# Kernel tuning notes

Measured on AMD Instinct MI355X. Metric: run time of the kernel, lower is better.

Reference implementation:

```python
import jax, jax.numpy as jnp
import numpy as np

B, DV, W, H = 64, 2048, 14, 14
DQ, DA, G, DH, NC = 2400, 1200, 2, 1200, 3000


def setup_inputs() -> dict:
    key = jax.random.key(0)
    ks = jax.random.split(key, 14)
    s = lambda k, shp, scale=0.02: jax.random.normal(k, shp, dtype=jnp.float32) * scale
    return {
        "input_q": jax.random.normal(ks[0], (B, DQ), dtype=jnp.float32),
        "input_v": jax.random.normal(ks[1], (B, DV, W, H), dtype=jnp.float32),
        "Wv_att": s(ks[2], (DA, DV)),
        "bv_att": s(ks[3], (DA,)),
        "Wq_att": s(ks[4], (DA, DQ)),
        "bq_att": s(ks[5], (DA,)),
        "Watt": s(ks[6], (G, DA)),
        "batt": s(ks[7], (G,)),
        "Wv_fus": s(ks[8], (G, DH, DV)),
        "bv_fus": s(ks[9], (G, DH)),
        "Wq_fus": s(ks[10], (G * DH, DQ)),
        "bq_fus": s(ks[11], (G * DH,)),
        "Wc": s(ks[12], (NC, G * DH)),
        "bc": s(ks[13], (NC,)),
    }


def reference(input_q, input_v, Wv_att, bv_att, Wq_att, bq_att, Watt, batt,
              Wv_fus, bv_fus, Wq_fus, bq_fus, Wc, bc):
    b, dv, w, h = input_v.shape
    n = w * h  # spatial positions

    # --- attention branch (eval mode: dropout = identity) ---
    # 1x1 conv == per-position linear over channels; activation_v = tanh
    xv = jnp.tanh(jnp.einsum('bchw,dc->bdhw', input_v, Wv_att) + bv_att[None, :, None, None])
    xv = xv.reshape(b, -1, n).transpose(0, 2, 1)               # [B, WH, DA]
    # question projection; activation_q = tanh
    xq = jnp.tanh(input_q @ Wq_att.T + bq_att)                 # [B, DA]
    # MLB Hadamard fusion + activation_mm = tanh
    xatt = jnp.tanh(xv * xq[:, None, :])                       # [B, WH, DA]
    # glimpse scores: 1x1 conv over dim_mm channels
    wgt = jnp.einsum('bnd,gd->bgn', xatt, Watt) + batt[None, :, None]  # [B, G, WH]
    att = jax.nn.softmax(wgt, axis=-1)                         # softmax over WH per glimpse

    # weighted sum of ORIGINAL features per glimpse
    v_flat = input_v.reshape(b, dv, n)                         # [B, DV, WH]
    v_att = jnp.einsum('bgn,bdn->bgd', att, v_flat)            # [B, G, DV]

    # --- glimpse fusion + classification ---
    v_fus = jnp.tanh(jnp.einsum('bgd,ghd->bgh', v_att, Wv_fus) + bv_fus)  # [B, G, DH]
    v_fus = v_fus.reshape(b, -1)                               # [B, G*DH] (concat over glimpses)
    q_fus = jnp.tanh(input_q @ Wq_fus.T + bq_fus)              # [B, G*DH]
    x = (v_fus * q_fus) @ Wc.T + bc                            # [B, NC]
    return (x, wgt)
```

## Files before the change

kernel.cpp:

```cpp
#include <hip/hip_runtime.h>
#include <hip/hip_fp16.h>

typedef _Float16 half8 __attribute__((ext_vector_type(8)));
typedef float f32x4 __attribute__((ext_vector_type(4)));

__device__ __forceinline__ float tanh_fast(float x) {
  float e = __expf(2.0f * x);
  return 1.0f - 2.0f / (e + 1.0f);
}

__device__ __forceinline__ void gload16(const _Float16* g, _Float16* l) {
  __builtin_amdgcn_global_load_lds((const __attribute__((address_space(1))) void*)g,
                                   (__attribute__((address_space(3))) void*)l,
                                   16, 0, 0);
}

__global__ __launch_bounds__(256) void k_transpose_v(const float* __restrict__ in,
                                                     _Float16* __restrict__ out) {
  __shared__ float t[64][65];
  int b = blockIdx.z;
  int c0 = blockIdx.y * 64;
  int p0 = blockIdx.x * 64;
  int tid = threadIdx.x;
  int pl = tid & 63;
  #pragma unroll
  for (int s = 0; s < 16; ++s) {
    int cl = (tid >> 6) + s * 4;
    int p = p0 + pl;
    t[cl][pl] = (p < 196) ? in[((size_t)b * 2048 + (c0 + cl)) * 196 + p] : 0.0f;
  }
  __syncthreads();
  int c8 = (tid & 7) * 8;
  #pragma unroll
  for (int s = 0; s < 2; ++s) {
    int p = p0 + (tid >> 3) + s * 32;
    if (p < 196) {
      half8 v;
      #pragma unroll
      for (int j = 0; j < 8; ++j) v[j] = (_Float16)t[c8 + j][(tid >> 3) + s * 32];
      *(half8*)(out + ((size_t)b * 196 + p) * 2048 + c0 + c8) = v;
    }
  }
}

__global__ __launch_bounds__(256) void k_prep(const float* __restrict__ W,
                                              _Float16* __restrict__ Wh,
                                              const float* __restrict__ batt,
                                              float* __restrict__ wgt) {
  int i = blockIdx.x * 256 + threadIdx.x;
  int n = i >> 11;
  Wh[i] = (n < 1200) ? (_Float16)W[i] : (_Float16)0.0f;
  if (i < 25088) wgt[i] = batt[(i / 196) & 1];
}

__global__ __launch_bounds__(256) void k_gemm1(const _Float16* __restrict__ A,
                                               const _Float16* __restrict__ B,
                                               const float* __restrict__ bias,
                                               const float* __restrict__ xq,
                                               const float* __restrict__ Watt,
                                               float* __restrict__ wgt) {
  __shared__ __align__(16) _Float16 As[128 * 64];
  __shared__ __align__(16) _Float16 Bs[128 * 64];
  int tid = threadIdx.x;
  int n0 = blockIdx.x * 128;
  int m0 = blockIdx.y * 128;
  int lane = tid & 63;
  int wave = tid >> 6;
  int wm = (wave >> 1) * 64;
  int wn = (wave & 1) * 64;
  int fr = lane & 15;
  int fq = lane >> 4;

  int rsub = lane >> 3;
  int gchunk = (lane & 7) ^ rsub;
  const _Float16* aSrc = A + (size_t)(m0 + wave * 8 + rsub) * 2048 + gchunk * 8;
  const _Float16* bSrc = B + (size_t)(n0 + wave * 8 + rsub) * 2048 + gchunk * 8;
  _Float16* aDst = As + (wave * 8) * 64;
  _Float16* bDst = Bs + (wave * 8) * 64;

  f32x4 acc[4][4];
  #pragma unroll
  for (int i = 0; i < 4; ++i)
    #pragma unroll
    for (int j = 0; j < 4; ++j) acc[i][j] = (f32x4){0.f, 0.f, 0.f, 0.f};

  for (int kt = 0; kt < 32; ++kt) {
    int k0 = kt * 64;
    __syncthreads();
    #pragma unroll
    for (int j = 0; j < 4; ++j) {
      gload16(aSrc + k0 + (size_t)j * 32 * 2048, aDst + j * 32 * 64);
      gload16(bSrc + k0 + (size_t)j * 32 * 2048, bDst + j * 32 * 64);
    }
    __syncthreads();
    #pragma unroll
    for (int s = 0; s < 2; ++s) {
      half8 af[4], bf[4];
      #pragma unroll
      for (int mt = 0; mt < 4; ++mt) {
        int row = wm + mt * 16 + fr;
        af[mt] = *(const half8*)(As + row * 64 + (((s * 4 + fq) ^ (fr & 7)) << 3));
      }
      #pragma unroll
      for (int nt = 0; nt < 4; ++nt) {
        int row = wn + nt * 16 + fr;
        bf[nt] = *(const half8*)(Bs + row * 64 + (((s * 4 + fq) ^ (fr & 7)) << 3));
      }
      #pragma unroll
      for (int mt = 0; mt < 4; ++mt)
        #pragma unroll
        for (int nt = 0; nt < 4; ++nt)
          acc[mt][nt] = __builtin_amdgcn_mfma_f32_16x16x32_f16(af[mt], bf[nt], acc[mt][nt], 0, 0, 0);
    }
  }

  float s0[16], s1[16];
  #pragma unroll
  for (int i = 0; i < 16; ++i) { s0[i] = 0.f; s1[i] = 0.f; }

  #pragma unroll
  for (int nt = 0; nt < 4; ++nt) {
    int col = n0 + wn + nt * 16 + fr;
    bool ok = col < 1200;
    float bcol = ok ? bias[col] : 0.f;
    float wa0 = ok ? Watt[col] : 0.f;
    float wa1 = ok ? Watt[1200 + col] : 0.f;
    #pragma unroll
    for (int mt = 0; mt < 4; ++mt) {
      #pragma unroll
      for (int r = 0; r < 4; ++r) {
        int row = m0 + wm + mt * 16 + fq * 4 + r;
        int b = row / 196;
        float xqv = ok ? xq[b * 1200 + col] : 0.f;
        float xv = tanh_fast(acc[mt][nt][r] + bcol);
        float xa = tanh_fast(xv * xqv);
        s0[mt * 4 + r] += xa * wa0;
        s1[mt * 4 + r] += xa * wa1;
      }
    }
  }
  #pragma unroll
  for (int i = 0; i < 16; ++i) {
    #pragma unroll
    for (int off = 8; off > 0; off >>= 1) {
      s0[i] += __shfl_down(s0[i], off);
      s1[i] += __shfl_down(s1[i], off);
    }
  }
  if (fr == 0) {
    #pragma unroll
    for (int i = 0; i < 16; ++i) {
      int row = m0 + wm + (i >> 2) * 16 + fq * 4 + (i & 3);
      int b = row / 196;
      int p = row - b * 196;
      atomicAdd(&wgt[(b * 2 + 0) * 196 + p], s0[i]);
      atomicAdd(&wgt[(b * 2 + 1) * 196 + p], s1[i]);
    }
  }
}

__global__ __launch_bounds__(64) void k_softmax(const float* __restrict__ wgt,
                                                float* __restrict__ att) {
  int bg = blockIdx.x;
  int lane = threadIdx.x;
  const float* wr = wgt + (size_t)bg * 196;
  float v[4];
  #pragma unroll
  for (int i = 0; i < 4; ++i) {
    int n = lane + i * 64;
    v[i] = (n < 196) ? wr[n] : -1e30f;
  }
  float mx = fmaxf(fmaxf(v[0], v[1]), fmaxf(v[2], v[3]));
  #pragma unroll
  for (int off = 32; off > 0; off >>= 1) mx = fmaxf(mx, __shfl_xor(mx, off));
  float s = 0.f;
  #pragma unroll
  for (int i = 0; i < 4; ++i) {
    int n = lane + i * 64;
    float e = (n < 196) ? __expf(v[i] - mx) : 0.f;
    v[i] = e;
    s += e;
  }
  #pragma unroll
  for (int off = 32; off > 0; off >>= 1) s += __shfl_xor(s, off);
  float inv = 1.f / s;
  #pragma unroll
  for (int i = 0; i < 4; ++i) {
    int n = lane + i * 64;
    if (n < 196) att[(size_t)bg * 196 + n] = v[i] * inv;
  }
}

__global__ __launch_bounds__(256) void k_vatt(const _Float16* __restrict__ Vt,
                                              const float* __restrict__ att,
                                              float* __restrict__ v_att) {
  __shared__ float a0s[196], a1s[196];
  int b = blockIdx.y;
  int tid = threadIdx.x;
  if (tid < 196) {
    a0s[tid] = att[((size_t)b * 2 + 0) * 196 + tid];
    a1s[tid] = att[((size_t)b * 2 + 1) * 196 + tid];
  }
  __syncthreads();
  int d = blockIdx.x * 256 + tid;
  const _Float16* vp = Vt + (size_t)b * 196 * 2048 + d;
  float s0 = 0.f, s1 = 0.f;
  for (int n = 0; n < 196; ++n) {
    float v = (float)vp[(size_t)n * 2048];
    s0 += a0s[n] * v;
    s1 += a1s[n] * v;
  }
  v_att[((size_t)b * 2 + 0) * 2048 + d] = s0;
  v_att[((size_t)b * 2 + 1) * 2048 + d] = s1;
}

__global__ __launch_bounds__(256) void k_skinny(const float* __restrict__ A1,
                                                const float* __restrict__ A2,
                                                int lda, int strideAz,
                                                const float* __restrict__ W, long strideWz,
                                                int N, int K, int S,
                                                float* __restrict__ P, int ldp, int colOffZ) {
  __shared__ __align__(16) float As[32][64];
  __shared__ __align__(16) float Ws2[32][64];
  int tid = threadIdx.x;
  int z = blockIdx.z;
  int s = blockIdx.y;
  int nt0 = blockIdx.x * 64;
  int tiles = K >> 5;
  int t0 = (s * tiles) / S;
  int t1 = ((s + 1) * tiles) / S;
  int tx = tid & 15, ty = tid >> 4;
  int lm = tid >> 2;
  int lk = (tid & 3) * 8;
  const float* Ab = A1 + (size_t)z * strideAz + (size_t)lm * lda;
  const float* A2b = A2 ? (A2 + (size_t)z * strideAz + (size_t)lm * lda) : nullptr;
  int ng = nt0 + lm;
  const float* Wb = W + (size_t)z * strideWz + (size_t)ng * K;
  bool wok = ng < N;
  float acc[4][4] = {};
  for (int t = t0; t < t1; ++t) {
    int k0 = t * 32;
    __syncthreads();
    #pragma unroll
    for (int j = 0; j < 8; ++j) {
      float v = Ab[k0 + lk + j];
      if (A2b) v *= A2b[k0 + lk + j];
      As[lk + j][lm] = v;
    }
    #pragma unroll
    for (int j = 0; j < 8; ++j) Ws2[lk + j][lm] = wok ? Wb[k0 + lk + j] : 0.0f;
    __syncthreads();
    #pragma unroll
    for (int kk = 0; kk < 32; ++kk) {
      f32x4 a = *(const f32x4*)&As[kk][ty * 4];
      f32x4 wv = *(const f32x4*)&Ws2[kk][tx * 4];
      #pragma unroll
      for (int i = 0; i < 4; ++i)
        #pragma unroll
        for (int j = 0; j < 4; ++j) acc[i][j] += a[i] * wv[j];
    }
  }
  #pragma unroll
  for (int i = 0; i < 4; ++i) {
    int m = ty * 4 + i;
    #pragma unroll
    for (int j = 0; j < 4; ++j) {
      int nl = nt0 + tx * 4 + j;
      if (nl < N) P[((size_t)s * 64 + m) * ldp + z * colOffZ + nl] = acc[i][j];
    }
  }
}

__global__ __launch_bounds__(256) void k_combine(const float* __restrict__ P, int S, int ldp,
                                                 const float* __restrict__ bias,
                                                 float* __restrict__ out, int total, int act) {
  int i = blockIdx.x * 256 + threadIdx.x;
  if (i >= total) return;
  int col = i % ldp;
  float sum = bias[col];
  for (int ss = 0; ss < S; ++ss) sum += P[(size_t)ss * total + i];
  out[i] = act ? tanh_fast(sum) : sum;
}

extern "C" void kernel_launch(void* const* d_in, const int* in_sizes, int n_in,
                              void* d_out, int out_size, void* d_ws, size_t ws_size,
                              hipStream_t stream) {
  const float* input_q = (const float*)d_in[0];
  const float* input_v = (const float*)d_in[1];
  const float* Wv_att  = (const float*)d_in[2];
  const float* bv_att  = (const float*)d_in[3];
  const float* Wq_att  = (const float*)d_in[4];
  const float* bq_att  = (const float*)d_in[5];
  const float* Watt    = (const float*)d_in[6];
  const float* batt    = (const float*)d_in[7];
  const float* Wv_fus  = (const float*)d_in[8];
  const float* bv_fus  = (const float*)d_in[9];
  const float* Wq_fus  = (const float*)d_in[10];
  const float* bq_fus  = (const float*)d_in[11];
  const float* Wc      = (const float*)d_in[12];
  const float* bc      = (const float*)d_in[13];
  float* out = (float*)d_out;

  char* ws = (char*)d_ws;
  _Float16* Vt   = (_Float16*)ws; ws += 51380224;
  _Float16* Wh   = (_Float16*)ws; ws += 5242880;
  float* xq      = (float*)ws;    ws += 307200;
  float* att     = (float*)ws;    ws += 100352;
  float* v_att   = (float*)ws;    ws += 1048576;
  float* v_fus   = (float*)ws;    ws += 614400;
  float* q_fus   = (float*)ws;    ws += 614400;
  float* P       = (float*)ws;    ws += 14745600;

  float* x_out   = out;
  float* wgt_out = out + 192000;

  const int S = 16;

  k_transpose_v<<<dim3(4, 32, 64), dim3(256), 0, stream>>>(input_v, Vt);
  k_prep<<<dim3(10240), dim3(256), 0, stream>>>(Wv_att, Wh, batt, wgt_out);

  k_skinny<<<dim3(19, S, 1), dim3(256), 0, stream>>>(input_q, nullptr, 2400, 0,
                                                     Wq_att, 0, 1200, 2400, S, P, 1200, 0);
  k_combine<<<dim3(300), dim3(256), 0, stream>>>(P, S, 1200, bq_att, xq, 76800, 1);

  k_skinny<<<dim3(38, S, 1), dim3(256), 0, stream>>>(input_q, nullptr, 2400, 0,
                                                     Wq_fus, 0, 2400, 2400, S, P + 1228800, 2400, 0);
  k_combine<<<dim3(600), dim3(256), 0, stream>>>(P + 1228800, S, 2400, bq_fus, q_fus, 153600, 1);

  k_gemm1<<<dim3(10, 98), dim3(256), 0, stream>>>(Vt, Wh, bv_att, xq, Watt, wgt_out);

  k_softmax<<<dim3(128), dim3(64), 0, stream>>>(wgt_out, att);

  k_vatt<<<dim3(8, 64), dim3(256), 0, stream>>>(Vt, att, v_att);

  k_skinny<<<dim3(19, S, 2), dim3(256), 0, stream>>>(v_att, nullptr, 4096, 2048,
                                                     Wv_fus, 1200L * 2048L, 1200, 2048, S, P, 2400, 1200);
  k_combine<<<dim3(600), dim3(256), 0, stream>>>(P, S, 2400, bv_fus, v_fus, 153600, 1);

  k_skinny<<<dim3(47, S, 1), dim3(256), 0, stream>>>(v_fus, q_fus, 2400, 0,
                                                     Wc, 0, 3000, 2400, S, P, 3000, 0);
  k_combine<<<dim3(750), dim3(256), 0, stream>>>(P, S, 3000, bc, x_out, 192000, 0);
}
```

Measured before the change: 514.7 us.

## Double-buffer gemm1 K-loop, fuse softmax into vatt and merge q projections

The attention GEMM now uses two 128x32 LDS buffers and prefetches the next K-slice with global_load_lds while computing the current one, synchronised by explicit waitcnt and barriers. The separate softmax kernel is folded into the v_att kernel, where each block recomputes the softmax for its batch row. The two question projections are merged into one skinny GEMM and one combine pass. The v_fus combine now also applies the q_fus Hadamard product so the classifier GEMM no longer needs a second operand. Together these cut launch count and aim to hide global-load latency in the main GEMM, at the cost of redundant softmax work across the 8 column blocks per batch and fragile hand-written wait counts.

Result: faster. 474.2 us (-7.9%).

```diff
diff --git a/kernel.cpp b/kernel.cpp
--- a/kernel.cpp
+++ b/kernel.cpp
@@ -59,8 +59,8 @@
                                                const float* __restrict__ xq,
                                                const float* __restrict__ Watt,
                                                float* __restrict__ wgt) {
-  __shared__ __align__(16) _Float16 As[128 * 64];
-  __shared__ __align__(16) _Float16 Bs[128 * 64];
+  __shared__ __align__(16) _Float16 As[2][128 * 32];
+  __shared__ __align__(16) _Float16 Bs[2][128 * 32];
   int tid = threadIdx.x;
   int n0 = blockIdx.x * 128;
   int m0 = blockIdx.y * 128;
@@ -71,12 +71,16 @@
   int fr = lane & 15;
   int fq = lane >> 4;
 
-  int rsub = lane >> 3;
-  int gchunk = (lane & 7) ^ rsub;
-  const _Float16* aSrc = A + (size_t)(m0 + wave * 8 + rsub) * 2048 + gchunk * 8;
-  const _Float16* bSrc = B + (size_t)(n0 + wave * 8 + rsub) * 2048 + gchunk * 8;
-  _Float16* aDst = As + (wave * 8) * 64;
-  _Float16* bDst = Bs + (wave * 8) * 64;
+  int rl = lane >> 2;
+  int cch = lane & 3;
+  int row0 = wave * 32 + rl;
+  int row1 = wave * 32 + 16 + rl;
+  int g0 = cch ^ ((row0 >> 1) & 3);
+  int g1 = cch ^ ((row1 >> 1) & 3);
+  const _Float16* aSrc0 = A + (size_t)(m0 + row0) * 2048 + g0 * 8;
+  const _Float16* aSrc1 = A + (size_t)(m0 + row1) * 2048 + g1 * 8;
+  const _Float16* bSrc0 = B + (size_t)(n0 + row0) * 2048 + g0 * 8;
+  const _Float16* bSrc1 = B + (size_t)(n0 + row1) * 2048 + g1 * 8;
 
   f32x4 acc[4][4];
   #pragma unroll
@@ -84,35 +88,44 @@
     #pragma unroll
     for (int j = 0; j < 4; ++j) acc[i][j] = (f32x4){0.f, 0.f, 0.f, 0.f};
 
-  for (int kt = 0; kt < 32; ++kt) {
-    int k0 = kt * 64;
-    __syncthreads();
-    #pragma unroll
-    for (int j = 0; j < 4; ++j) {
-      gload16(aSrc + k0 + (size_t)j * 32 * 2048, aDst + j * 32 * 64);
-      gload16(bSrc + k0 + (size_t)j * 32 * 2048, bDst + j * 32 * 64);
-    }
-    __syncthreads();
-    #pragma unroll
-    for (int s = 0; s < 2; ++s) {
-      half8 af[4], bf[4];
+  auto stage = [&](int buf, int k0) {
+    _Float16* dA = &As[buf][(wave * 32) * 32];
+    _Float16* dB = &Bs[buf][(wave * 32) * 32];
+    gload16(aSrc0 + k0, dA);
+    gload16(aSrc1 + k0, dA + 16 * 32);
+    gload16(bSrc0 + k0, dB);
+    gload16(bSrc1 + k0, dB + 16 * 32);
+  };
+  int sw = (fr >> 1) & 3;
+  auto compute = [&](int buf) {
+    half8 af[4], bf[4];
+    #pragma unroll
+    for (int mt = 0; mt < 4; ++mt)
+      af[mt] = *(const half8*)(&As[buf][(wm + mt * 16 + fr) * 32 + ((fq ^ sw) << 3)]);
+    #pragma unroll
+    for (int nt = 0; nt < 4; ++nt)
+      bf[nt] = *(const half8*)(&Bs[buf][(wn + nt * 16 + fr) * 32 + ((fq ^ sw) << 3)]);
+    #pragma unroll
+    for (int mt = 0; mt < 4; ++mt)
       #pragma unroll
-      for (int mt = 0; mt < 4; ++mt) {
-        int row = wm + mt * 16 + fr;
-        af[mt] = *(const half8*)(As + row * 64 + (((s * 4 + fq) ^ (fr & 7)) << 3));
-      }
-      #pragma unroll
-      for (int nt = 0; nt < 4; ++nt) {
-        int row = wn + nt * 16 + fr;
-        bf[nt] = *(const half8*)(Bs + row * 64 + (((s * 4 + fq) ^ (fr & 7)) << 3));
-      }
-      #pragma unroll
-      for (int mt = 0; mt < 4; ++mt)
-        #pragma unroll
-        for (int nt = 0; nt < 4; ++nt)
-          acc[mt][nt] = __builtin_amdgcn_mfma_f32_16x16x32_f16(af[mt], bf[nt], acc[mt][nt], 0, 0, 0);
-    }
-  }
+      for (int nt = 0; nt < 4; ++nt)
+        acc[mt][nt] = __builtin_amdgcn_mfma_f32_16x16x32_f16(af[mt], bf[nt], acc[mt][nt], 0, 0, 0);
+  };
+
+  stage(0, 0);
+  stage(1, 32);
+  for (int kt = 0; kt < 63; ++kt) {
+    int cur = kt & 1;
+    asm volatile("s_waitcnt vmcnt(4)" ::: "memory");
+    __builtin_amdgcn_s_barrier();
+    compute(cur);
+    asm volatile("s_waitcnt lgkmcnt(0)" ::: "memory");
+    __builtin_amdgcn_s_barrier();
+    if (kt < 62) stage(cur, (kt + 2) * 32);
+  }
+  asm volatile("s_waitcnt vmcnt(0)" ::: "memory");
+  __builtin_amdgcn_s_barrier();
+  compute(1);
 
   float s0[16], s1[16];
   #pragma unroll
@@ -159,47 +172,41 @@
   }
 }
 
-__global__ __launch_bounds__(64) void k_softmax(const float* __restrict__ wgt,
-                                                float* __restrict__ att) {
-  int bg = blockIdx.x;
-  int lane = threadIdx.x;
-  const float* wr = wgt + (size_t)bg * 196;
-  float v[4];
-  #pragma unroll
-  for (int i = 0; i < 4; ++i) {
-    int n = lane + i * 64;
-    v[i] = (n < 196) ? wr[n] : -1e30f;
-  }
-  float mx = fmaxf(fmaxf(v[0], v[1]), fmaxf(v[2], v[3]));
-  #pragma unroll
-  for (int off = 32; off > 0; off >>= 1) mx = fmaxf(mx, __shfl_xor(mx, off));
-  float s = 0.f;
-  #pragma unroll
-  for (int i = 0; i < 4; ++i) {
-    int n = lane + i * 64;
-    float e = (n < 196) ? __expf(v[i] - mx) : 0.f;
-    v[i] = e;
-    s += e;
-  }
-  #pragma unroll
-  for (int off = 32; off > 0; off >>= 1) s += __shfl_xor(s, off);
-  float inv = 1.f / s;
-  #pragma unroll
-  for (int i = 0; i < 4; ++i) {
-    int n = lane + i * 64;
-    if (n < 196) att[(size_t)bg * 196 + n] = v[i] * inv;
-  }
-}
-
 __global__ __launch_bounds__(256) void k_vatt(const _Float16* __restrict__ Vt,
-                                              const float* __restrict__ att,
+                                              const float* __restrict__ wgt,
                                               float* __restrict__ v_att) {
   __shared__ float a0s[196], a1s[196];
   int b = blockIdx.y;
   int tid = threadIdx.x;
-  if (tid < 196) {
-    a0s[tid] = att[((size_t)b * 2 + 0) * 196 + tid];
-    a1s[tid] = att[((size_t)b * 2 + 1) * 196 + tid];
+  int wv = tid >> 6, lane = tid & 63;
+  if (wv < 2) {
+    const float* wr = wgt + ((size_t)b * 2 + wv) * 196;
+    float v[4];
+    #pragma unroll
+    for (int i = 0; i < 4; ++i) {
+      int n = lane + i * 64;
+      v[i] = (n < 196) ? wr[n] : -1e30f;
+    }
+    float mx = fmaxf(fmaxf(v[0], v[1]), fmaxf(v[2], v[3]));
+    #pragma unroll
+    for (int off = 32; off > 0; off >>= 1) mx = fmaxf(mx, __shfl_xor(mx, off));
+    float s = 0.f;
+    #pragma unroll
+    for (int i = 0; i < 4; ++i) {
+      int n = lane + i * 64;
+      float e = (n < 196) ? __expf(v[i] - mx) : 0.f;
+      v[i] = e;
+      s += e;
+    }
+    #pragma unroll
+    for (int off = 32; off > 0; off >>= 1) s += __shfl_xor(s, off);
+    float inv = 1.f / s;
+    float* dst = wv ? a1s : a0s;
+    #pragma unroll
+    for (int i = 0; i < 4; ++i) {
+      int n = lane + i * 64;
+      if (n < 196) dst[n] = v[i] * inv;
+    }
   }
   __syncthreads();
   int d = blockIdx.x * 256 + tid;
@@ -212,6 +219,75 @@
   }
   v_att[((size_t)b * 2 + 0) * 2048 + d] = s0;
   v_att[((size_t)b * 2 + 1) * 2048 + d] = s1;
+}
+
+__global__ __launch_bounds__(256) void k_skinnyQ(const float* __restrict__ q,
+                                                 const float* __restrict__ Wa,
+                                                 const float* __restrict__ Wf,
+                                                 int S, float* __restrict__ P) {
+  __shared__ __align__(16) float As[32][64];
+  __shared__ __align__(16) float Ws2[32][64];
+  int tid = threadIdx.x;
+  int x = blockIdx.x;
+  int s = blockIdx.y;
+  bool f = x >= 19;
+  const float* W = f ? Wf : Wa;
+  int nt0 = f ? (x - 19) * 64 : x * 64;
+  int N = f ? 2400 : 1200;
+  int colBase = f ? 1200 : 0;
+  const int K = 2400;
+  int tiles = K >> 5;
+  int t0 = (s * tiles) / S;
+  int t1 = ((s + 1) * tiles) / S;
+  int tx = tid & 15, ty = tid >> 4;
+  int lm = tid >> 2;
+  int lk = (tid & 3) * 8;
+  const float* Ab = q + (size_t)lm * K;
+  int ng = nt0 + lm;
+  const float* Wb = W + (size_t)ng * K;
+  bool wok = ng < N;
+  float acc[4][4] = {};
+  for (int t = t0; t < t1; ++t) {
+    int k0 = t * 32;
+    __syncthreads();
+    #pragma unroll
+    for (int j = 0; j < 8; ++j) As[lk + j][lm] = Ab[k0 + lk + j];
+    #pragma unroll
+    for (int j = 0; j < 8; ++j) Ws2[lk + j][lm] = wok ? Wb[k0 + lk + j] : 0.0f;
+    __syncthreads();
+    #pragma unroll
+    for (int kk = 0; kk < 32; ++kk) {
+      f32x4 a = *(const f32x4*)&As[kk][ty * 4];
+      f32x4 wv = *(const f32x4*)&Ws2[kk][tx * 4];
+      #pragma unroll
+      for (int i = 0; i < 4; ++i)
+        #pragma unroll
+        for (int j = 0; j < 4; ++j) acc[i][j] += a[i] * wv[j];
+    }
+  }
+  #pragma unroll
+  for (int i = 0; i < 4; ++i) {
+    int m = ty * 4 + i;
+    #pragma unroll
+    for (int j = 0; j < 4; ++j) {
+      int nl = nt0 + tx * 4 + j;
+      if (nl < N) P[((size_t)s * 64 + m) * 3600 + colBase + nl] = acc[i][j];
+    }
+  }
+}
+
+__global__ __launch_bounds__(256) void k_combineQ(const float* __restrict__ P, int S,
+                                                  const float* __restrict__ bq_att,
+                                                  const float* __restrict__ bq_fus,
+                                                  float* __restrict__ xq,
+                                                  float* __restrict__ q_fus) {
+  int i = blockIdx.x * 256 + threadIdx.x;
+  if (i >= 230400) return;
+  int row = i / 3600, col = i % 3600;
+  float sum = 0.f;
+  for (int ss = 0; ss < S; ++ss) sum += P[(size_t)ss * 230400 + i];
+  if (col < 1200) xq[row * 1200 + col] = tanh_fast(sum + bq_att[col]);
+  else            q_fus[row * 2400 + col - 1200] = tanh_fast(sum + bq_fus[col - 1200]);
 }
 
 __global__ __launch_bounds__(256) void k_skinny(const float* __restrict__ A1,
@@ -271,15 +347,26 @@
   }
 }
 
+__global__ __launch_bounds__(256) void k_combineVh(const float* __restrict__ P, int S,
+                                                   const float* __restrict__ bv_fus,
+                                                   const float* __restrict__ q_fus,
+                                                   float* __restrict__ h) {
+  int i = blockIdx.x * 256 + threadIdx.x;
+  if (i >= 153600) return;
+  int col = i % 2400;
+  float sum = bv_fus[col];
+  for (int ss = 0; ss < S; ++ss) sum += P[(size_t)ss * 153600 + i];
+  h[i] = tanh_fast(sum) * q_fus[i];
+}
+
 __global__ __launch_bounds__(256) void k_combine(const float* __restrict__ P, int S, int ldp,
                                                  const float* __restrict__ bias,
-                                                 float* __restrict__ out, int total, int act) {
+                                                 float* __restrict__ out, int total) {
   int i = blockIdx.x * 256 + threadIdx.x;
   if (i >= total) return;
-  int col = i % ldp;
-  float sum = bias[col];
+  float sum = bias[i % ldp];
   for (int ss = 0; ss < S; ++ss) sum += P[(size_t)ss * total + i];
-  out[i] = act ? tanh_fast(sum) : sum;
+  out[i] = sum;
 }
 
 extern "C" void kernel_launch(void* const* d_in, const int* in_sizes, int n_in,
@@ -305,7 +392,6 @@
   _Float16* Vt   = (_Float16*)ws; ws += 51380224;
   _Float16* Wh   = (_Float16*)ws; ws += 5242880;
   float* xq      = (float*)ws;    ws += 307200;
-  float* att     = (float*)ws;    ws += 100352;
   float* v_att   = (float*)ws;    ws += 1048576;
   float* v_fus   = (float*)ws;    ws += 614400;
   float* q_fus   = (float*)ws;    ws += 614400;
@@ -319,25 +405,18 @@
   k_transpose_v<<<dim3(4, 32, 64), dim3(256), 0, stream>>>(input_v, Vt);
   k_prep<<<dim3(10240), dim3(256), 0, stream>>>(Wv_att, Wh, batt, wgt_out);
 
-  k_skinny<<<dim3(19, S, 1), dim3(256), 0, stream>>>(input_q, nullptr, 2400, 0,
-                                                     Wq_att, 0, 1200, 2400, S, P, 1200, 0);
-  k_combine<<<dim3(300), dim3(256), 0, stream>>>(P, S, 1200, bq_att, xq, 76800, 1);
-
-  k_skinny<<<dim3(38, S, 1), dim3(256), 0, stream>>>(input_q, nullptr, 2400, 0,
-                                                     Wq_fus, 0, 2400, 2400, S, P + 1228800, 2400, 0);
-  k_combine<<<dim3(600), dim3(256), 0, stream>>>(P + 1228800, S, 2400, bq_fus, q_fus, 153600, 1);
+  k_skinnyQ<<<dim3(57, S), dim3(256), 0, stream>>>(input_q, Wq_att, Wq_fus, S, P);
+  k_combineQ<<<dim3(900), dim3(256), 0, stream>>>(P, S, bq_att, bq_fus, xq, q_fus);
 
   k_gemm1<<<dim3(10, 98), dim3(256), 0, stream>>>(Vt, Wh, bv_att, xq, Watt, wgt_out);
 
-  k_softmax<<<dim3(128), dim3(64), 0, stream>>>(wgt_out, att);
-
-  k_vatt<<<dim3(8, 64), dim3(256), 0, stream>>>(Vt, att, v_att);
+  k_vatt<<<dim3(8, 64), dim3(256), 0, stream>>>(Vt, wgt_out, v_att);
 
   k_skinny<<<dim3(19, S, 2), dim3(256), 0, stream>>>(v_att, nullptr, 4096, 2048,
                                                      Wv_fus, 1200L * 2048L, 1200, 2048, S, P, 2400, 1200);
-  k_combine<<<dim3(600), dim3(256), 0, stream>>>(P, S, 2400, bv_fus, v_fus, 153600, 1);
-
-  k_skinny<<<dim3(47, S, 1), dim3(256), 0, stream>>>(v_fus, q_fus, 2400, 0,
+  k_combineVh<<<dim3(600), dim3(256), 0, stream>>>(P, S, bv_fus, q_fus, v_fus);
+
+  k_skinny<<<dim3(47, S, 1), dim3(256), 0, stream>>>(v_fus, nullptr, 2400, 0,
                                                      Wc, 0, 3000, 2400, S, P, 3000, 0);
-  k_combine<<<dim3(750), dim3(256), 0, stream>>>(P, S, 3000, bc, x_out, 192000, 0);
-}
+  k_combine<<<dim3(750), dim3(256), 0, stream>>>(P, S, 3000, bc, x_out, 192000);
+}
```
